# Kernel tuning notes

Measured on AMD Instinct MI355X. Metric: run time of the kernel, lower is better.

The kernel has to match this reference:

```python
import jax, jax.numpy as jnp
import numpy as np

NUM_CLASSES = 80
STRIDES = (8, 16, 32)


def _decode(p, stride):
    # p: [B, 5+C, H, W] raw head -> [B, HW, 5+C] decoded (xy in px, wh=exp*stride)
    B, C, H, W = p.shape
    ys, xs = jnp.meshgrid(jnp.arange(H), jnp.arange(W), indexing='ij')
    grid = jnp.stack([xs, ys], -1).reshape(H * W, 2).astype(p.dtype)
    out = p.reshape(B, C, H * W).transpose(0, 2, 1)
    xy = (out[..., :2] + grid) * stride
    wh = jnp.exp(out[..., 2:4]) * stride
    out = jnp.concatenate([xy, wh, out[..., 4:]], -1)
    es = jnp.full((H * W,), float(stride), p.dtype)
    return out, grid[:, 0], grid[:, 1], es


def _pairwise_iou(gt, pr):
    # gt [G,4] cxcywh, pr [A,4] -> [G,A]
    gt_tl = gt[:, None, :2] - gt[:, None, 2:] * 0.5
    gt_br = gt[:, None, :2] + gt[:, None, 2:] * 0.5
    pr_tl = pr[None, :, :2] - pr[None, :, 2:] * 0.5
    pr_br = pr[None, :, :2] + pr[None, :, 2:] * 0.5
    tl = jnp.maximum(gt_tl, pr_tl)
    br = jnp.minimum(gt_br, pr_br)
    en = jnp.all(tl < br, -1).astype(gt.dtype)
    inter = jnp.prod(br - tl, -1) * en
    a_gt = jnp.prod(gt[:, 2:], -1)[:, None]
    a_pr = jnp.prod(pr[:, 2:], -1)[None, :]
    return inter / (a_gt + a_pr - inter + 1e-16)


def _assign(gt_boxes, gt_cls, bbox, clsp, objp, xg, yg, es):
    # SimOTA assignment for one image (all fixed-shape; non-candidate anchors
    # are masked out via huge cost instead of boolean gather).
    G = gt_boxes.shape[0]
    xc = (xg + 0.5) * es  # [A] anchor centers
    yc = (yg + 0.5) * es
    gl = gt_boxes[:, 0:1] - 0.5 * gt_boxes[:, 2:3]
    gr = gt_boxes[:, 0:1] + 0.5 * gt_boxes[:, 2:3]
    gt_ = gt_boxes[:, 1:2] - 0.5 * gt_boxes[:, 3:4]
    gb = gt_boxes[:, 1:2] + 0.5 * gt_boxes[:, 3:4]
    in_box = (xc[None] > gl) & (xc[None] < gr) & (yc[None] > gt_) & (yc[None] < gb)  # [G,A]
    r = 2.5 * es[None]
    in_ctr = ((xc[None] > gt_boxes[:, 0:1] - r) & (xc[None] < gt_boxes[:, 0:1] + r)
              & (yc[None] > gt_boxes[:, 1:2] - r) & (yc[None] < gt_boxes[:, 1:2] + r))
    fg_cand = jnp.any(in_box, 0) | jnp.any(in_ctr, 0)  # [A]
    in_both = in_box & in_ctr  # [G,A]

    ious = _pairwise_iou(gt_boxes, bbox)  # [G,A]
    ious_m = jnp.where(fg_cand[None, :], ious, 0.0)
    iou_cost = -jnp.log(ious_m + 1e-8)

    # pairwise cls BCE cost: bce(sqrt(sigmoid(cls)*sigmoid(obj)), onehot(gt)).sum(-1)
    p = jnp.sqrt(jax.nn.sigmoid(clsp) * jax.nn.sigmoid(objp[:, None]))  # [A,C]
    lp = jnp.maximum(jnp.log(p), -100.0)
    l1p = jnp.maximum(jnp.log1p(-p), -100.0)
    t = jax.nn.one_hot(gt_cls, NUM_CLASSES, dtype=p.dtype)  # [G,C]
    cls_cost = -(jnp.einsum('ac,gc->ga', lp - l1p, t) + jnp.sum(l1p, -1)[None, :])

    cost = (cls_cost + 3.0 * iou_cost
            + 1e5 * (~in_both).astype(p.dtype)
            + 1e9 * (~fg_cand)[None, :].astype(p.dtype))

    # dynamic-k: k_g = clamp(sum(top10 ious), min=1)
    topk_ious, _ = jax.lax.top_k(ious_m, 10)
    dyn_k = jnp.clip(topk_ious.sum(-1).astype(jnp.int32), 1, None)  # [G]
    rank = jnp.argsort(jnp.argsort(cost, axis=1), axis=1)  # rank of each anchor per gt
    matching = (rank < dyn_k[:, None]) & fg_cand[None, :]  # [G,A]
    # resolve anchors matched to multiple gts: keep min-cost gt
    multi = matching.sum(0) > 1
    best = jnp.argmin(cost, 0)
    matching = jnp.where(multi[None, :], jnp.arange(G)[:, None] == best[None, :], matching)

    fg = jnp.any(matching, 0)  # [A]
    matched_gt = jnp.argmax(matching, 0)  # [A]
    pred_iou = jnp.sum(matching * ious, 0)  # [A]
    matched_cls = gt_cls[matched_gt]
    return fg, matched_gt, pred_iou, matched_cls


def _giou_loss(b, g):
    tl = jnp.maximum(b[..., :2] - b[..., 2:] * 0.5, g[..., :2] - g[..., 2:] * 0.5)
    br = jnp.minimum(b[..., :2] + b[..., 2:] * 0.5, g[..., :2] + g[..., 2:] * 0.5)
    area_b = jnp.prod(b[..., 2:], -1)
    area_g = jnp.prod(g[..., 2:], -1)
    en = jnp.all(tl < br, -1).astype(b.dtype)
    inter = jnp.prod(br - tl, -1) * en
    union = area_b + area_g - inter
    iou = inter / (union + 1e-16)
    ctl = jnp.minimum(b[..., :2] - b[..., 2:] * 0.5, g[..., :2] - g[..., 2:] * 0.5)
    cbr = jnp.maximum(b[..., :2] + b[..., 2:] * 0.5, g[..., :2] + g[..., 2:] * 0.5)
    area_c = jnp.maximum(jnp.prod(cbr - ctl, -1), 1e-16)
    giou = iou - (area_c - union) / area_c
    return 1.0 - jnp.clip(giou, -1.0, 1.0)


def _bce_logits(x, t):
    return jnp.maximum(x, 0.0) - x * t + jnp.log1p(jnp.exp(-jnp.abs(x)))


def _forward(p8, p16, p32, labels):
    outs, xo, yo, eo = [], [], [], []
    for p, s in zip((p8, p16, p32), STRIDES):
        o, x, y, e = _decode(p, s)
        outs.append(o); xo.append(x); yo.append(y); eo.append(e)
    outputs = jnp.concatenate(outs, 1)  # [B, A, 5+C]
    xg = jnp.concatenate(xo); yg = jnp.concatenate(yo); es = jnp.concatenate(eo)

    bbox = outputs[..., :4]
    obj = outputs[..., 4]
    cls = outputs[..., 5:]
    gt_boxes = labels[..., :4]
    gt_cls = labels[..., 4].astype(jnp.int32)

    # assignment runs under no_grad in torch
    det = jax.lax.stop_gradient(outputs)
    fg, matched_gt, pred_iou, matched_cls = jax.vmap(
        lambda gb, gc, o: _assign(gb, gc, o[..., :4], o[..., 5:], o[..., 4], xg, yg, es)
    )(gt_boxes, gt_cls, det)

    fgf = fg.astype(outputs.dtype)  # [B,A]
    reg_t = jnp.take_along_axis(gt_boxes, matched_gt[..., None], axis=1)  # [B,A,4]
    cls_t = (jax.nn.one_hot(matched_cls, NUM_CLASSES, dtype=outputs.dtype)
             * pred_iou[..., None] * fgf[..., None])

    loss_iou = jnp.sum(_giou_loss(bbox, reg_t) * fgf)
    loss_obj = jnp.sum(_bce_logits(obj, fgf))
    loss_cls = jnp.sum(_bce_logits(cls, cls_t) * fgf[..., None])
    num_fg = jnp.maximum(jnp.sum(fgf), 1.0)
    return (5.0 * loss_iou + loss_obj + loss_cls) / num_fg


def setup_inputs() -> dict:
    key = jax.random.key(0)
    k1, k2, k3, k4, k5, k6 = jax.random.split(key, 6)
    B, NGT = 32, 20
    p8 = jax.random.normal(k1, (B, 5 + NUM_CLASSES, 80, 80), dtype=jnp.float32)
    p16 = jax.random.normal(k2, (B, 5 + NUM_CLASSES, 40, 40), dtype=jnp.float32)
    p32 = jax.random.normal(k3, (B, 5 + NUM_CLASSES, 20, 20), dtype=jnp.float32)
    cxy = jax.random.uniform(k4, (B, NGT, 2), dtype=jnp.float32, minval=32.0, maxval=608.0)
    wh = jax.random.uniform(k5, (B, NGT, 2), dtype=jnp.float32, minval=16.0, maxval=128.0)
    cls = jax.random.randint(k6, (B, NGT, 1), 0, NUM_CLASSES).astype(jnp.float32)
    labels = jnp.concatenate([cxy, wh, cls], -1)
    return {"p8": p8, "p16": p16, "p32": p32, "labels": labels}


def reference(p8, p16, p32, labels):
    return _forward(p8, p16, p32, labels)
```

## Files before the change

### kernel.cpp

```cpp
#include <hip/hip_runtime.h>
#include <cstdint>
#include <cstddef>

#define NA 8400
#define NAP 8448
#define NB 32
#define NG 20
#define NCL 80
#define NBLK 33
#define KC_BLKS 12

__device__ __forceinline__ float frcp(float x) { return __builtin_amdgcn_rcpf(x); }
__device__ __forceinline__ float bce0(float x) {
  return fmaxf(x, 0.0f) + __logf(1.0f + __expf(-fabsf(x)));
}

__device__ __forceinline__ void anchor_info(int a, const float* p8, const float* p16,
                                            const float* p32, int b, const float*& base,
                                            int& hw, int& HW, int& xg, int& yg, float& fs) {
  if (a < 6400)      { hw = a;        HW = 6400; xg = hw % 80; yg = hw / 80; fs = 8.f;
                       base = p8  + (size_t)b * 85 * 6400; }
  else if (a < 8000) { hw = a - 6400; HW = 1600; xg = hw % 40; yg = hw / 40; fs = 16.f;
                       base = p16 + (size_t)b * 85 * 1600; }
  else               { hw = a - 8000; HW = 400;  xg = hw % 20; yg = hw / 20; fs = 32.f;
                       base = p32 + (size_t)b * 85 * 400; }
}

__device__ __forceinline__ float iou_raw(float gx, float gy, float gw, float gh, float4 p) {
  float gtlx = gx - gw * 0.5f, gtly = gy - gh * 0.5f;
  float gbrx = gx + gw * 0.5f, gbry = gy + gh * 0.5f;
  float ptlx = p.x - p.z * 0.5f, ptly = p.y - p.w * 0.5f;
  float pbrx = p.x + p.z * 0.5f, pbry = p.y + p.w * 0.5f;
  float tlx = fmaxf(gtlx, ptlx), tly = fmaxf(gtly, ptly);
  float brx = fminf(gbrx, pbrx), bry = fminf(gbry, pbry);
  float inter = ((tlx < brx) && (tly < bry)) ? (brx - tlx) * (bry - tly) : 0.0f;
  float ag = gw * gh, ap = p.z * p.w;
  return inter * frcp(ag + ap - inter + 1e-16f);
}

__device__ __forceinline__ float giou_loss(float4 bb, float gx, float gy, float gw, float gh) {
  float btlx = bb.x - bb.z * 0.5f, btly = bb.y - bb.w * 0.5f;
  float bbrx = bb.x + bb.z * 0.5f, bbry = bb.y + bb.w * 0.5f;
  float gtlx = gx - gw * 0.5f, gtly = gy - gh * 0.5f;
  float gbrx = gx + gw * 0.5f, gbry = gy + gh * 0.5f;
  float tlx = fmaxf(btlx, gtlx), tly = fmaxf(btly, gtly);
  float brx = fminf(bbrx, gbrx), bry = fminf(bbry, gbry);
  float area_b = bb.z * bb.w, area_g = gw * gh;
  float inter = ((tlx < brx) && (tly < bry)) ? (brx - tlx) * (bry - tly) : 0.0f;
  float uni = area_b + area_g - inter;
  float iou = inter / (uni + 1e-16f);
  float ctlx = fminf(btlx, gtlx), ctly = fminf(btly, gtly);
  float cbrx = fmaxf(bbrx, gbrx), cbry = fmaxf(bbry, gbry);
  float area_c = fmaxf((cbrx - ctlx) * (cbry - ctly), 1e-16f);
  float giou = iou - (area_c - uni) / area_c;
  giou = fminf(fmaxf(giou, -1.0f), 1.0f);
  return 1.0f - giou;
}

__device__ __forceinline__ void block_argmin(float& v, int& i, volatile float* s_v,
                                             volatile int* s_i, int tid) {
#pragma unroll
  for (int off = 32; off; off >>= 1) {
    float ov = __shfl_down(v, off, 64);
    int   oi = __shfl_down(i, off, 64);
    if (ov < v || (ov == v && oi < i)) { v = ov; i = oi; }
  }
  if ((tid & 63) == 0) { s_v[tid >> 6] = v; s_i[tid >> 6] = i; }
  __syncthreads();
  v = s_v[0]; i = s_i[0];
#pragma unroll
  for (int w = 1; w < 4; ++w) {
    float ov = s_v[w]; int oi = s_i[w];
    if (ov < v || (ov == v && oi < i)) { v = ov; i = oi; }
  }
}

__global__ __launch_bounds__(256) void kGXA(const float* __restrict__ p8,
                                            const float* __restrict__ p16,
                                            const float* __restrict__ p32,
                                            const float* __restrict__ labels,
                                            int* __restrict__ n_fg_cnt,
                                            int* __restrict__ fg_list,
                                            unsigned int* __restrict__ am_c,
                                            float4* __restrict__ bbox_c,
                                            float* __restrict__ sl_c,
                                            float* __restrict__ sb_c,
                                            float* __restrict__ w_c,
                                            unsigned int* __restrict__ match_c,
                                            float* __restrict__ blk_obj) {
  __shared__ float s_gt[NG * 4];
  __shared__ unsigned int s_gmask[NCL];
  __shared__ unsigned int s_wcnt[4];
  __shared__ float s_part[4];
  __shared__ unsigned int s_base;
  int blk = blockIdx.x, b = blockIdx.y, tid = threadIdx.x, lane = tid & 63, wid = tid >> 6;

  if (tid < NCL) s_gmask[tid] = 0u;
  if (tid < NG) {
    s_gt[tid * 4 + 0] = labels[((size_t)b * NG + tid) * 5 + 0];
    s_gt[tid * 4 + 1] = labels[((size_t)b * NG + tid) * 5 + 1];
    s_gt[tid * 4 + 2] = labels[((size_t)b * NG + tid) * 5 + 2];
    s_gt[tid * 4 + 3] = labels[((size_t)b * NG + tid) * 5 + 3];
  }
  __syncthreads();
  if (tid < NG) {
    int c = (int)labels[((size_t)b * NG + tid) * 5 + 4];
    atomicOr(&s_gmask[c], 1u << tid);
  }
  __syncthreads();

  int a = blk * 256 + tid;
  match_c[(size_t)b * NAP + a] = 0u;

  bool fg = false;
  unsigned int msk = 0u;
  float bce_obj = 0.0f, obj = 0.0f;
  const float* base = nullptr; int hw = 0, HW = 0, xg = 0, yg = 0; float fs = 8.f;
  if (a < NA) {
    anchor_info(a, p8, p16, p32, b, base, hw, HW, xg, yg, fs);
    obj = base[4 * HW + hw];
    bce_obj = bce0(obj);
    float xc = ((float)xg + 0.5f) * fs;
    float yc = ((float)yg + 0.5f) * fs;
    float r = 2.5f * fs;
#pragma unroll
    for (int g = 0; g < NG; ++g) {
      float gx = s_gt[g * 4 + 0], gy = s_gt[g * 4 + 1];
      float gw = s_gt[g * 4 + 2], gh = s_gt[g * 4 + 3];
      bool inb = (xc > gx - 0.5f * gw) && (xc < gx + 0.5f * gw) &&
                 (yc > gy - 0.5f * gh) && (yc < gy + 0.5f * gh);
      bool inc = (xc > gx - r) && (xc < gx + r) && (yc > gy - r) && (yc < gy + r);
      fg = fg || inb || inc;
      if (inb && inc) msk |= (1u << g);
    }
  }

  unsigned long long bm = __ballot(fg);
#pragma unroll
  for (int off = 32; off; off >>= 1) bce_obj += __shfl_down(bce_obj, off, 64);
  if (lane == 0) { s_wcnt[wid] = (unsigned int)__popcll(bm); s_part[wid] = bce_obj; }
  __syncthreads();
  if (tid == 0) {
    unsigned int cnt = s_wcnt[0] + s_wcnt[1] + s_wcnt[2] + s_wcnt[3];
    s_base = cnt ? (unsigned int)atomicAdd(&n_fg_cnt[b], (int)cnt) : 0u;
    blk_obj[b * NBLK + blk] = s_part[0] + s_part[1] + s_part[2] + s_part[3];
  }
  __syncthreads();

  if (!fg) return;
  unsigned int pos = s_base;
  for (int w = 0; w < wid; ++w) pos += s_wcnt[w];
  pos += (unsigned int)__popcll(bm & ((1ull << lane) - 1ull));
  int ci = (int)pos;
  size_t bo = (size_t)b * NAP;
  fg_list[bo + ci] = a;
  am_c[bo + ci] = msk | 0x80000000u;

  float v0 = base[hw];
  float v1 = base[HW + hw];
  float v2 = base[2 * HW + hw];
  float v3 = base[3 * HW + hw];
  bbox_c[bo + ci] = make_float4((v0 + (float)xg) * fs, (v1 + (float)yg) * fs,
                                __expf(v2) * fs, __expf(v3) * fs);
  float uo  = __logf(1.0f + __expf(-fabsf(obj)));
  float lso = fminf(obj, 0.0f) - uo;

  float sl = 0.0f, sb = 0.0f;
  for (int cc = 0; cc < NCL; cc += 8) {
    float xs[8];
#pragma unroll
    for (int j = 0; j < 8; ++j) xs[j] = base[(5 + cc + j) * HW + hw];
#pragma unroll
    for (int j = 0; j < 8; ++j) {
      float x = xs[j];
      float u = __logf(1.0f + __expf(-fabsf(x)));
      sb += fmaxf(x, 0.0f) + u;
      float lsx = fminf(x, 0.0f) - u;
      float lpr = 0.5f * (lsx + lso);
      float p   = __expf(lpr);
      float l1p = fmaxf(__logf(1.0f - p), -100.0f);
      sl += l1p;
      unsigned int m = s_gmask[cc + j];
      if (m) {
        float w = fmaxf(lpr, -100.0f) - l1p;
        do {
          int g = __ffs(m) - 1; m &= m - 1;
          w_c[((size_t)b * NG + g) * NAP + ci] = w;
        } while (m);
      }
    }
  }
  sl_c[bo + ci] = sl;
  sb_c[bo + ci] = sb;
}

__global__ __launch_bounds__(256) void kB(const float* __restrict__ labels,
                                          const float4* __restrict__ bbox_c,
                                          const float* __restrict__ sl_c,
                                          const float* __restrict__ w_c,
                                          const unsigned int* __restrict__ am_c,
                                          const int* __restrict__ n_fg,
                                          unsigned int* __restrict__ match_c) {
  __shared__ float s_cost[NAP];
  __shared__ float s_wt[4 * 10];
  __shared__ float s_v[4];
  __shared__ int   s_i[4];
  __shared__ int   s_k;

  int g = blockIdx.x, b = blockIdx.y, tid = threadIdx.x;
  int lane = tid & 63, wid = tid >> 6;
  int n = n_fg[b];
  size_t bo = (size_t)b * NAP;
  const float* __restrict__ wg = w_c + ((size_t)b * NG + g) * NAP;

  float gx = labels[((size_t)b * NG + g) * 5 + 0];
  float gy = labels[((size_t)b * NG + g) * 5 + 1];
  float gw = labels[((size_t)b * NG + g) * 5 + 2];
  float gh = labels[((size_t)b * NG + g) * 5 + 3];

  float t10[10];
#pragma unroll
  for (int j = 0; j < 10; ++j) t10[j] = 0.0f;

  for (int ci = tid; ci < n; ci += 256) {
    unsigned int am = am_c[bo + ci];
    float wv = wg[ci];
    float sl = sl_c[bo + ci];
    float4 pb = bbox_c[bo + ci];
    float iou = iou_raw(gx, gy, gw, gh, pb);
    if (iou > t10[9]) {
      t10[9] = iou;
#pragma unroll
      for (int q = 9; q > 0; --q) {
        if (t10[q] > t10[q - 1]) { float t = t10[q]; t10[q] = t10[q - 1]; t10[q - 1] = t; }
        else break;
      }
    }
    float c = -(wv + sl) - 3.0f * __logf(iou + 1e-8f);
    if (!((am >> g) & 1u)) c += 100000.0f;
    s_cost[ci] = c;
  }

  for (int r = 0; r < 10; ++r) {
    float v = t10[0];
    float bv = v;
#pragma unroll
    for (int off = 32; off; off >>= 1) bv = fmaxf(bv, __shfl_down(bv, off, 64));
    bv = __shfl(bv, 0, 64);
    unsigned long long won = __ballot(v == bv);
    if (lane == __ffsll(won) - 1) {
#pragma unroll
      for (int q = 0; q < 9; ++q) t10[q] = t10[q + 1];
      t10[9] = -1.0f;
    }
    if (lane == 0) s_wt[wid * 10 + r] = bv;
  }
  __syncthreads();

  if (tid == 0) {
    int p0 = 0, p1 = 0, p2 = 0, p3 = 0;
    float s = 0.0f;
    for (int r = 0; r < 10; ++r) {
      float v0 = (p0 < 10) ? s_wt[p0]      : -2.0f;
      float v1 = (p1 < 10) ? s_wt[10 + p1] : -2.0f;
      float v2 = (p2 < 10) ? s_wt[20 + p2] : -2.0f;
      float v3 = (p3 < 10) ? s_wt[30 + p3] : -2.0f;
      float m = fmaxf(fmaxf(v0, v1), fmaxf(v2, v3));
      s += m;
      if (m == v0) ++p0; else if (m == v1) ++p1; else if (m == v2) ++p2; else ++p3;
    }
    int k = (int)s;
    if (k < 1) k = 1;
    s_k = k;
  }
  __syncthreads();
  int k = s_k;

  for (int it = 0; it < k; ++it) {
    float bv = 3.4e38f; int bi = NAP;
    for (int ci = tid; ci < n; ci += 256) {
      float v = s_cost[ci];
      if (v < bv || (v == bv && ci < bi)) { bv = v; bi = ci; }
    }
    block_argmin(bv, bi, s_v, s_i, tid);
    if (bv >= 1e8f) break;
    if (tid == 0) {
      atomicOr(&match_c[bo + bi], 1u << g);
      s_cost[bi] = 3.4e38f;
    }
    __syncthreads();
  }
}

__global__ __launch_bounds__(256) void kCD(const float* __restrict__ p8,
                                           const float* __restrict__ p16,
                                           const float* __restrict__ p32,
                                           const float* __restrict__ labels,
                                           const float4* __restrict__ bbox_c,
                                           const float* __restrict__ sl_c,
                                           const float* __restrict__ sb_c,
                                           const float* __restrict__ w_c,
                                           const unsigned int* __restrict__ am_c,
                                           const int* __restrict__ fg_list,
                                           const int* __restrict__ n_fg,
                                           const unsigned int* __restrict__ match_c,
                                           const float* __restrict__ blk_obj,
                                           float* __restrict__ accum,
                                           int* __restrict__ done_cnt,
                                           float* __restrict__ out) {
  __shared__ float s_gt[NG * 5];
  __shared__ float s_red[16];
  __shared__ int s_last;
  int b = blockIdx.y, tid = threadIdx.x;
  if (tid < NG * 5) s_gt[tid] = labels[(size_t)b * NG * 5 + tid];
  __syncthreads();

  int n = n_fg[b];
  size_t bo = (size_t)b * NAP;
  float li = 0.0f, oe = 0.0f, lc = 0.0f, nf = 0.0f;

  for (int ci = blockIdx.x * 256 + tid; ci < n; ci += KC_BLKS * 256) {
    unsigned int m = match_c[bo + ci];
    if (m == 0u) continue;
    int a = fg_list[bo + ci];
    const float* base; int hw, HW, xg, yg; float fs;
    anchor_info(a, p8, p16, p32, b, base, hw, HW, xg, yg, fs);
    float4 pb = bbox_c[bo + ci];
    int mg;
    if (m & (m - 1)) {
      unsigned int am = am_c[bo + ci];
      float sl = sl_c[bo + ci];
      float bestc = 3.4e38f; mg = 0;
#pragma unroll 4
      for (int g = 0; g < NG; ++g) {
        float iou = iou_raw(s_gt[g * 5], s_gt[g * 5 + 1], s_gt[g * 5 + 2], s_gt[g * 5 + 3], pb);
        float wv = w_c[((size_t)b * NG + g) * NAP + ci];
        float c = -(wv + sl) - 3.0f * __logf(iou + 1e-8f);
        if (!((am >> g) & 1u)) c += 100000.0f;
        if (c < bestc) { bestc = c; mg = g; }
      }
    } else {
      mg = __ffs(m) - 1;
    }
    float gx = s_gt[mg * 5], gy = s_gt[mg * 5 + 1];
    float gw = s_gt[mg * 5 + 2], gh = s_gt[mg * 5 + 3];
    int cg = (int)s_gt[mg * 5 + 4];
    float piou = iou_raw(gx, gy, gw, gh, pb);
    li += giou_loss(pb, gx, gy, gw, gh);
    float xcls = base[(5 + cg) * HW + hw];
    lc += sb_c[bo + ci] - xcls * piou;
    oe += base[4 * HW + hw];
    nf += 1.0f;
  }

  float vals[4] = {li, oe, lc, nf};
#pragma unroll
  for (int q = 0; q < 4; ++q) {
#pragma unroll
    for (int off = 32; off; off >>= 1) vals[q] += __shfl_down(vals[q], off, 64);
  }
  if ((tid & 63) == 0) {
    int wid = tid >> 6;
    s_red[wid * 4 + 0] = vals[0];
    s_red[wid * 4 + 1] = vals[1];
    s_red[wid * 4 + 2] = vals[2];
    s_red[wid * 4 + 3] = vals[3];
  }
  __syncthreads();
  if (tid < 4) {
    const int slot[4] = {0, 2, 3, 4};
    float s = s_red[tid] + s_red[4 + tid] + s_red[8 + tid] + s_red[12 + tid];
    atomicAdd(&accum[slot[tid]], s);
  }

  if (tid == 0) {
    __threadfence();
    int old = atomicAdd(done_cnt, 1);
    s_last = (old == KC_BLKS * NB - 1) ? 1 : 0;
  }
  __syncthreads();
  if (s_last) {
    float s = 0.0f;
    for (int i = tid; i < NB * NBLK; i += 256) s += blk_obj[i];
#pragma unroll
    for (int off = 32; off; off >>= 1) s += __shfl_down(s, off, 64);
    if ((tid & 63) == 0) s_red[tid >> 6] = s;
    __syncthreads();
    if (tid == 0) {
      float obj_base = s_red[0] + s_red[1] + s_red[2] + s_red[3];
      float loss_iou = atomicAdd(&accum[0], 0.0f);
      float oex      = atomicAdd(&accum[2], 0.0f);
      float loss_cls = atomicAdd(&accum[3], 0.0f);
      float num_fg   = atomicAdd(&accum[4], 0.0f);
      float loss_obj = obj_base - oex;
      out[0] = (5.0f * loss_iou + loss_obj + loss_cls) / fmaxf(num_fg, 1.0f);
    }
  }
}

extern "C" void kernel_launch(void* const* d_in, const int* in_sizes, int n_in,
                              void* d_out, int out_size, void* d_ws, size_t ws_size,
                              hipStream_t stream) {
  const float* p8     = (const float*)d_in[0];
  const float* p16    = (const float*)d_in[1];
  const float* p32    = (const float*)d_in[2];
  const float* labels = (const float*)d_in[3];
  float* out = (float*)d_out;

  const size_t BAP = (size_t)NB * NAP;
  char* w = (char*)d_ws;
  float4*       bbox_c  = (float4*)w;
  float*        w_c     = (float*)(w + BAP * 16);
  char*         w2      = w + BAP * 16 + (size_t)NB * NG * NAP * 4;
  int*          fg_list = (int*)(w2);
  unsigned int* am_c    = (unsigned int*)(w2 + BAP * 4);
  unsigned int* match_c = (unsigned int*)(w2 + BAP * 8);
  float*        sl_c    = (float*)(w2 + BAP * 12);
  float*        sb_c    = (float*)(w2 + BAP * 16);
  char*         w3      = w2 + BAP * 20;
  int*          n_fg    = (int*)w3;
  float*        accum   = (float*)(w3 + 128);
  int*          done_cnt= (int*)(w3 + 160);
  float*        blk_obj = (float*)(w3 + 256);

  hipMemsetAsync(w3, 0, 256, stream);

  kGXA<<<dim3(NBLK, NB), dim3(256), 0, stream>>>(p8, p16, p32, labels, n_fg, fg_list, am_c,
                                                 bbox_c, sl_c, sb_c, w_c, match_c, blk_obj);
  kB<<<dim3(NG, NB), dim3(256), 0, stream>>>(labels, bbox_c, sl_c, w_c, am_c, n_fg, match_c);
  kCD<<<dim3(KC_BLKS, NB), dim3(256), 0, stream>>>(p8, p16, p32, labels, bbox_c, sl_c, sb_c,
                                                   w_c, am_c, fg_list, n_fg, match_c, blk_obj,
                                                   accum, done_cnt, out);
}
```

Before: 181.7 us.

## Precompute full per-GT cost and IoU tables in first kernel, compact fg threads

The first kernel now compacts foreground anchors within each block through shared memory, so the costly per-anchor class loop runs on dense lanes instead of divergent ones. It also computes, for every GT, the complete SimOTA cost and IoU and writes them as [G,A] tables. The top-k kernel and the final loss kernel then read these values instead of recomputing IoU, log and masks. The trade-off is a second G-sized table to write and the loss of the sparse class-mask write path; every GT now writes a cost entry for every candidate.

```diff
diff --git a/kernel.cpp b/kernel.cpp
--- a/kernel.cpp
+++ b/kernel.cpp
@@ -81,31 +81,29 @@
                                             const float* __restrict__ labels,
                                             int* __restrict__ n_fg_cnt,
                                             int* __restrict__ fg_list,
-                                            unsigned int* __restrict__ am_c,
                                             float4* __restrict__ bbox_c,
-                                            float* __restrict__ sl_c,
                                             float* __restrict__ sb_c,
-                                            float* __restrict__ w_c,
+                                            float* __restrict__ cost_tbl,
+                                            float* __restrict__ iou_tbl,
                                             unsigned int* __restrict__ match_c,
                                             float* __restrict__ blk_obj) {
   __shared__ float s_gt[NG * 4];
-  __shared__ unsigned int s_gmask[NCL];
+  __shared__ int   s_gcls[NG];
+  __shared__ int   s_a[256];
+  __shared__ unsigned int s_msk[256];
+  __shared__ float s_lso[256];
   __shared__ unsigned int s_wcnt[4];
   __shared__ float s_part[4];
   __shared__ unsigned int s_base;
+  __shared__ int s_c;
   int blk = blockIdx.x, b = blockIdx.y, tid = threadIdx.x, lane = tid & 63, wid = tid >> 6;
 
-  if (tid < NCL) s_gmask[tid] = 0u;
   if (tid < NG) {
     s_gt[tid * 4 + 0] = labels[((size_t)b * NG + tid) * 5 + 0];
     s_gt[tid * 4 + 1] = labels[((size_t)b * NG + tid) * 5 + 1];
     s_gt[tid * 4 + 2] = labels[((size_t)b * NG + tid) * 5 + 2];
     s_gt[tid * 4 + 3] = labels[((size_t)b * NG + tid) * 5 + 3];
-  }
-  __syncthreads();
-  if (tid < NG) {
-    int c = (int)labels[((size_t)b * NG + tid) * 5 + 4];
-    atomicOr(&s_gmask[c], 1u << tid);
+    s_gcls[tid] = (int)labels[((size_t)b * NG + tid) * 5 + 4];
   }
   __syncthreads();
 
@@ -115,8 +113,8 @@
   bool fg = false;
   unsigned int msk = 0u;
   float bce_obj = 0.0f, obj = 0.0f;
-  const float* base = nullptr; int hw = 0, HW = 0, xg = 0, yg = 0; float fs = 8.f;
   if (a < NA) {
+    const float* base; int hw, HW, xg, yg; float fs;
     anchor_info(a, p8, p16, p32, b, base, hw, HW, xg, yg, fs);
     obj = base[4 * HW + hw];
     bce_obj = bce0(obj);
@@ -142,28 +140,40 @@
   __syncthreads();
   if (tid == 0) {
     unsigned int cnt = s_wcnt[0] + s_wcnt[1] + s_wcnt[2] + s_wcnt[3];
+    s_c = (int)cnt;
     s_base = cnt ? (unsigned int)atomicAdd(&n_fg_cnt[b], (int)cnt) : 0u;
     blk_obj[b * NBLK + blk] = s_part[0] + s_part[1] + s_part[2] + s_part[3];
   }
-  __syncthreads();
-
-  if (!fg) return;
-  unsigned int pos = s_base;
-  for (int w = 0; w < wid; ++w) pos += s_wcnt[w];
-  pos += (unsigned int)__popcll(bm & ((1ull << lane) - 1ull));
-  int ci = (int)pos;
+  if (fg) {
+    unsigned int li = 0;
+    for (int w = 0; w < wid; ++w) li += s_wcnt[w];
+    li += (unsigned int)__popcll(bm & ((1ull << lane) - 1ull));
+    s_a[li] = a;
+    s_msk[li] = msk;
+    float uo = __logf(1.0f + __expf(-fabsf(obj)));
+    s_lso[li] = fminf(obj, 0.0f) - uo;
+  }
+  __syncthreads();
+
+  int c = s_c;
+  if (tid >= c) return;
+  int ci = (int)s_base + tid;
   size_t bo = (size_t)b * NAP;
-  fg_list[bo + ci] = a;
-  am_c[bo + ci] = msk | 0x80000000u;
+  int aa = s_a[tid];
+  unsigned int mk = s_msk[tid];
+  float lso = s_lso[tid];
+
+  const float* base; int hw, HW, xg, yg; float fs;
+  anchor_info(aa, p8, p16, p32, b, base, hw, HW, xg, yg, fs);
+  fg_list[bo + ci] = aa;
 
   float v0 = base[hw];
   float v1 = base[HW + hw];
   float v2 = base[2 * HW + hw];
   float v3 = base[3 * HW + hw];
-  bbox_c[bo + ci] = make_float4((v0 + (float)xg) * fs, (v1 + (float)yg) * fs,
-                                __expf(v2) * fs, __expf(v3) * fs);
-  float uo  = __logf(1.0f + __expf(-fabsf(obj)));
-  float lso = fminf(obj, 0.0f) - uo;
+  float4 pb = make_float4((v0 + (float)xg) * fs, (v1 + (float)yg) * fs,
+                          __expf(v2) * fs, __expf(v3) * fs);
+  bbox_c[bo + ci] = pb;
 
   float sl = 0.0f, sb = 0.0f;
   for (int cc = 0; cc < NCL; cc += 8) {
@@ -178,27 +188,31 @@
       float lsx = fminf(x, 0.0f) - u;
       float lpr = 0.5f * (lsx + lso);
       float p   = __expf(lpr);
-      float l1p = fmaxf(__logf(1.0f - p), -100.0f);
-      sl += l1p;
-      unsigned int m = s_gmask[cc + j];
-      if (m) {
-        float w = fmaxf(lpr, -100.0f) - l1p;
-        do {
-          int g = __ffs(m) - 1; m &= m - 1;
-          w_c[((size_t)b * NG + g) * NAP + ci] = w;
-        } while (m);
-      }
-    }
-  }
-  sl_c[bo + ci] = sl;
+      sl += fmaxf(__logf(1.0f - p), -100.0f);
+    }
+  }
   sb_c[bo + ci] = sb;
-}
-
-__global__ __launch_bounds__(256) void kB(const float* __restrict__ labels,
-                                          const float4* __restrict__ bbox_c,
-                                          const float* __restrict__ sl_c,
-                                          const float* __restrict__ w_c,
-                                          const unsigned int* __restrict__ am_c,
+
+  for (int g = 0; g < NG; ++g) {
+    int cg = s_gcls[g];
+    float x = base[(5 + cg) * HW + hw];
+    float u = __logf(1.0f + __expf(-fabsf(x)));
+    float lsx = fminf(x, 0.0f) - u;
+    float lpr = 0.5f * (lsx + lso);
+    float p   = __expf(lpr);
+    float l1p = fmaxf(__logf(1.0f - p), -100.0f);
+    float wv  = fmaxf(lpr, -100.0f) - l1p;
+    float iou = iou_raw(s_gt[g * 4 + 0], s_gt[g * 4 + 1], s_gt[g * 4 + 2], s_gt[g * 4 + 3], pb);
+    float cst = -(wv + sl) - 3.0f * __logf(iou + 1e-8f);
+    if (!((mk >> g) & 1u)) cst += 100000.0f;
+    size_t row = ((size_t)b * NG + g) * NAP + ci;
+    cost_tbl[row] = cst;
+    iou_tbl[row]  = iou;
+  }
+}
+
+__global__ __launch_bounds__(256) void kB(const float* __restrict__ cost_tbl,
+                                          const float* __restrict__ iou_tbl,
                                           const int* __restrict__ n_fg,
                                           unsigned int* __restrict__ match_c) {
   __shared__ float s_cost[NAP];
@@ -211,23 +225,16 @@
   int lane = tid & 63, wid = tid >> 6;
   int n = n_fg[b];
   size_t bo = (size_t)b * NAP;
-  const float* __restrict__ wg = w_c + ((size_t)b * NG + g) * NAP;
-
-  float gx = labels[((size_t)b * NG + g) * 5 + 0];
-  float gy = labels[((size_t)b * NG + g) * 5 + 1];
-  float gw = labels[((size_t)b * NG + g) * 5 + 2];
-  float gh = labels[((size_t)b * NG + g) * 5 + 3];
+  const float* __restrict__ cg = cost_tbl + ((size_t)b * NG + g) * NAP;
+  const float* __restrict__ ig = iou_tbl  + ((size_t)b * NG + g) * NAP;
 
   float t10[10];
 #pragma unroll
   for (int j = 0; j < 10; ++j) t10[j] = 0.0f;
 
   for (int ci = tid; ci < n; ci += 256) {
-    unsigned int am = am_c[bo + ci];
-    float wv = wg[ci];
-    float sl = sl_c[bo + ci];
-    float4 pb = bbox_c[bo + ci];
-    float iou = iou_raw(gx, gy, gw, gh, pb);
+    float iou = ig[ci];
+    float cst = cg[ci];
     if (iou > t10[9]) {
       t10[9] = iou;
 #pragma unroll
@@ -236,9 +243,7 @@
         else break;
       }
     }
-    float c = -(wv + sl) - 3.0f * __logf(iou + 1e-8f);
-    if (!((am >> g) & 1u)) c += 100000.0f;
-    s_cost[ci] = c;
+    s_cost[ci] = cst;
   }
 
   for (int r = 0; r < 10; ++r) {
@@ -297,10 +302,9 @@
                                            const float* __restrict__ p32,
                                            const float* __restrict__ labels,
                                            const float4* __restrict__ bbox_c,
-                                           const float* __restrict__ sl_c,
                                            const float* __restrict__ sb_c,
-                                           const float* __restrict__ w_c,
-                                           const unsigned int* __restrict__ am_c,
+                                           const float* __restrict__ cost_tbl,
+                                           const float* __restrict__ iou_tbl,
                                            const int* __restrict__ fg_list,
                                            const int* __restrict__ n_fg,
                                            const unsigned int* __restrict__ match_c,
@@ -322,30 +326,25 @@
   for (int ci = blockIdx.x * 256 + tid; ci < n; ci += KC_BLKS * 256) {
     unsigned int m = match_c[bo + ci];
     if (m == 0u) continue;
+    int mg;
+    if (m & (m - 1)) {
+      float bestc = 3.4e38f; mg = 0;
+#pragma unroll 4
+      for (int g = 0; g < NG; ++g) {
+        float cst = cost_tbl[((size_t)b * NG + g) * NAP + ci];
+        if (cst < bestc) { bestc = cst; mg = g; }
+      }
+    } else {
+      mg = __ffs(m) - 1;
+    }
     int a = fg_list[bo + ci];
     const float* base; int hw, HW, xg, yg; float fs;
     anchor_info(a, p8, p16, p32, b, base, hw, HW, xg, yg, fs);
     float4 pb = bbox_c[bo + ci];
-    int mg;
-    if (m & (m - 1)) {
-      unsigned int am = am_c[bo + ci];
-      float sl = sl_c[bo + ci];
-      float bestc = 3.4e38f; mg = 0;
-#pragma unroll 4
-      for (int g = 0; g < NG; ++g) {
-        float iou = iou_raw(s_gt[g * 5], s_gt[g * 5 + 1], s_gt[g * 5 + 2], s_gt[g * 5 + 3], pb);
-        float wv = w_c[((size_t)b * NG + g) * NAP + ci];
-        float c = -(wv + sl) - 3.0f * __logf(iou + 1e-8f);
-        if (!((am >> g) & 1u)) c += 100000.0f;
-        if (c < bestc) { bestc = c; mg = g; }
-      }
-    } else {
-      mg = __ffs(m) - 1;
-    }
     float gx = s_gt[mg * 5], gy = s_gt[mg * 5 + 1];
     float gw = s_gt[mg * 5 + 2], gh = s_gt[mg * 5 + 3];
     int cg = (int)s_gt[mg * 5 + 4];
-    float piou = iou_raw(gx, gy, gw, gh, pb);
+    float piou = iou_tbl[((size_t)b * NG + mg) * NAP + ci];
     li += giou_loss(pb, gx, gy, gw, gh);
     float xcls = base[(5 + cg) * HW + hw];
     lc += sb_c[bo + ci] - xcls * piou;
@@ -409,26 +408,26 @@
 
   const size_t BAP = (size_t)NB * NAP;
   char* w = (char*)d_ws;
-  float4*       bbox_c  = (float4*)w;
-  float*        w_c     = (float*)(w + BAP * 16);
-  char*         w2      = w + BAP * 16 + (size_t)NB * NG * NAP * 4;
-  int*          fg_list = (int*)(w2);
-  unsigned int* am_c    = (unsigned int*)(w2 + BAP * 4);
-  unsigned int* match_c = (unsigned int*)(w2 + BAP * 8);
-  float*        sl_c    = (float*)(w2 + BAP * 12);
-  float*        sb_c    = (float*)(w2 + BAP * 16);
-  char*         w3      = w2 + BAP * 20;
-  int*          n_fg    = (int*)w3;
-  float*        accum   = (float*)(w3 + 128);
-  int*          done_cnt= (int*)(w3 + 160);
-  float*        blk_obj = (float*)(w3 + 256);
+  float4*       bbox_c   = (float4*)w;
+  float*        cost_tbl = (float*)(w + BAP * 16);
+  float*        iou_tbl  = cost_tbl + (size_t)NB * NG * NAP;
+  char*         w2       = (char*)(iou_tbl + (size_t)NB * NG * NAP);
+  int*          fg_list  = (int*)(w2);
+  unsigned int* match_c  = (unsigned int*)(w2 + BAP * 4);
+  float*        sb_c     = (float*)(w2 + BAP * 8);
+  char*         w3       = w2 + BAP * 12;
+  int*          n_fg     = (int*)w3;
+  float*        accum    = (float*)(w3 + 128);
+  int*          done_cnt = (int*)(w3 + 160);
+  float*        blk_obj  = (float*)(w3 + 256);
 
   hipMemsetAsync(w3, 0, 256, stream);
 
-  kGXA<<<dim3(NBLK, NB), dim3(256), 0, stream>>>(p8, p16, p32, labels, n_fg, fg_list, am_c,
-                                                 bbox_c, sl_c, sb_c, w_c, match_c, blk_obj);
-  kB<<<dim3(NG, NB), dim3(256), 0, stream>>>(labels, bbox_c, sl_c, w_c, am_c, n_fg, match_c);
-  kCD<<<dim3(KC_BLKS, NB), dim3(256), 0, stream>>>(p8, p16, p32, labels, bbox_c, sl_c, sb_c,
-                                                   w_c, am_c, fg_list, n_fg, match_c, blk_obj,
-                                                   accum, done_cnt, out);
-}
+  kGXA<<<dim3(NBLK, NB), dim3(256), 0, stream>>>(p8, p16, p32, labels, n_fg, fg_list,
+                                                 bbox_c, sb_c, cost_tbl, iou_tbl,
+                                                 match_c, blk_obj);
+  kB<<<dim3(NG, NB), dim3(256), 0, stream>>>(cost_tbl, iou_tbl, n_fg, match_c);
+  kCD<<<dim3(KC_BLKS, NB), dim3(256), 0, stream>>>(p8, p16, p32, labels, bbox_c, sb_c,
+                                                   cost_tbl, iou_tbl, fg_list, n_fg,
+                                                   match_c, blk_obj, accum, done_cnt, out);
+}
```

Result: no change. 181.2 us (-0.3%).
